# Optimization experiments

Measured on AMD Instinct MI355X. Metric: run time of the kernel, lower is better.

Reference implementation:

```python
import jax, jax.numpy as jnp
import numpy as np

N_FILTERS = 1024
KH, KW = 5, 5
LOC = 3                      # locality (pad + maxpool kernel/stride)
B, H, W = 1024, 64, 64
WIN = KH + 2 * LOC           # 11: sliced window side after padding


def setup_inputs() -> dict:
    key = jax.random.key(0)
    k1, k2, k3, k4 = jax.random.split(key, 4)
    X = jax.random.normal(k1, (B, 1, H, W), dtype=jnp.float32)
    weight = jax.random.normal(k2, (N_FILTERS, 1, KH, KW), dtype=jnp.float32)
    bias = jax.random.normal(k3, (N_FILTERS,), dtype=jnp.float32)
    # top-left corner (i, j) of each filter's window in the padded image;
    # must satisfy i + KH + 2*LOC <= H + 2*LOC  =>  i in [0, H-KH]
    positions = jax.random.randint(k4, (N_FILTERS, 2), 0, H - KH + 1, dtype=jnp.int32)
    return {"X": X, "weight": weight, "bias": bias, "positions": positions}


def reference(X, weight, bias, positions):
    # ZeroPad2d(locality)
    Xp = jnp.pad(X, ((0, 0), (0, 0), (LOC, LOC), (LOC, LOC)))

    def slice_one(pos):
        return jax.lax.dynamic_slice(Xp, (0, 0, pos[0], pos[1]), (B, 1, WIN, WIN))

    windows = jax.vmap(slice_one)(positions)
    lhs = jnp.transpose(windows[:, :, 0], (1, 0, 2, 3))

    # All n_filters tiny single-channel convs as ONE grouped conv.
    conv = jax.lax.conv_general_dilated(
        lhs, weight, window_strides=(1, 1), padding='VALID',
        dimension_numbers=('NCHW', 'OIHW', 'NCHW'),
        feature_group_count=N_FILTERS)                # [B,F,2L+1,2L+1] = [B,F,7,7]
    conv = conv + bias[None, :, None, None]

    # MaxPool2d((LOC,LOC)) with default stride=LOC, floor mode -> 2x2.
    pooled = jax.lax.reduce_window(
        conv, -jnp.inf, jax.lax.max,
        window_dimensions=(1, 1, LOC, LOC),
        window_strides=(1, 1, LOC, LOC),
        padding='VALID')                              # [B,F,2,2]

    # torch.cat(dim=1) over per-filter [B,1,2,2] tensors + reshape(B,-1)
    return pooled.reshape(B, -1)                      # [B, F*4]
```

## Files before the change

### kernel.cpp

```cpp
#include <hip/hip_runtime.h>

#define N_FILTERS 1024
#define B_TOTAL   1024
#define IMG       64
#define PAD_DIM   70

typedef _Float16 half2_t __attribute__((ext_vector_type(2)));
typedef float    fvec2  __attribute__((ext_vector_type(2)));

__global__ void zero_border_kernel(_Float16* __restrict__ Xt) {
    int bid = blockIdx.x;
    int r, c;
    if (bid < 420) {
        int r6 = bid / 70;
        c = bid - r6 * 70;
        r = (r6 < 3) ? r6 : r6 + 64;
    } else {
        int t = bid - 420;
        r = 3 + t / 6;
        int k = t - (t / 6) * 6;
        c = (k < 3) ? k : k + 64;
    }
    const size_t pp = (size_t)r * PAD_DIM + c;
    const int bg = threadIdx.x >> 5, l = threadIdx.x & 31;
    unsigned long long* q = (unsigned long long*)Xt
        + (size_t)bg * (4900ull * 32) + pp * 32 + l;
    *q = 0ull;
}

__global__ __launch_bounds__(256) void transpose_kernel(
    const float* __restrict__ X, _Float16* __restrict__ Xt)
{
    __shared__ float T[64 * 65];
    const int pt = blockIdx.x & 63;
    const int bt = blockIdx.x >> 6;
    const int tx = threadIdx.x & 63, ty = threadIdx.x >> 6;

    #pragma unroll
    for (int pass = 0; pass < 16; ++pass) {
        int bl = pass * 4 + ty;
        T[bl * 65 + tx] = X[(size_t)(bt * 64 + bl) * 4096 + pt * 64 + tx];
    }
    __syncthreads();
    #pragma unroll
    for (int pass = 0; pass < 16; ++pass) {
        int pl = pass * 4 + ty;
        int p  = pt * 64 + pl;
        int r  = p >> 6, c = p & 63;
        Xt[((size_t)(bt >> 1) * 4900 + (size_t)(r + 3) * PAD_DIM + (c + 3)) * 128
           + (bt & 1) * 64 + tx] = (_Float16)T[tx * 65 + pl];
    }
}

__global__ __launch_bounds__(256, 4) void filters_main(
    const half2_t* __restrict__ Xt2,
    const float*   __restrict__ W,
    const float*   __restrict__ bias,
    const int*     __restrict__ pos,
    float4*        __restrict__ out4)
{
    const int t    = threadIdx.x;
    const int lane = t & 63;
    const int w    = t >> 6;
    const int bg   = blockIdx.x & 7;
    const int fg   = blockIdx.x >> 3;

    const int f  = fg * 4 + w;
    const int sf = __builtin_amdgcn_readfirstlane(f);
    const int si = __builtin_amdgcn_readfirstlane(pos[2 * sf]);
    const int sj = __builtin_amdgcn_readfirstlane(pos[2 * sf + 1]);

    float wk[25];
    const float* wp = W + sf * 25;
    #pragma unroll
    for (int k = 0; k < 25; ++k) wk[k] = wp[k];

    const half2_t* Xg = Xt2 + (size_t)bg * (4900ull * 64) + lane;

    fvec2 acc[36];
    #pragma unroll
    for (int k = 0; k < 36; ++k) acc[k] = (fvec2)0.0f;

    #pragma unroll
    for (int wr = 0; wr < 10; ++wr) {
        const half2_t* rowp = Xg + (size_t)((si + wr) * PAD_DIM + sj) * 64;
        const int ylo = (wr > 4) ? (wr - 4) : 0;
        const int yhi = (wr < 5) ? wr : 5;
        #pragma unroll
        for (int wc = 0; wc < 10; ++wc) {
            half2_t h = rowp[wc * 64];
            fvec2 v;
            v.x = (float)h.x;
            v.y = (float)h.y;
            const int xlo = (wc > 4) ? (wc - 4) : 0;
            const int xhi = (wc < 5) ? wc : 5;
            #pragma unroll
            for (int y = 0; y < 6; ++y) {
                if (y >= ylo && y <= yhi) {
                    const int r = wr - y;
                    #pragma unroll
                    for (int x = 0; x < 6; ++x) {
                        if (x >= xlo && x <= xhi) {
                            const int c = wc - x;
                            acc[y * 6 + x] = wk[r * 5 + c] * v + acc[y * 6 + x];
                        }
                    }
                }
            }
        }
    }

    const float bv = bias[sf];
    float4 oA, oB;
    {
        float mA[4], mB[4];
        #pragma unroll
        for (int py = 0; py < 2; ++py) {
            #pragma unroll
            for (int px = 0; px < 2; ++px) {
                fvec2 m = acc[(3 * py) * 6 + 3 * px];
                #pragma unroll
                for (int dy = 0; dy < 3; ++dy)
                    #pragma unroll
                    for (int dx = 0; dx < 3; ++dx) {
                        fvec2 v = acc[(3 * py + dy) * 6 + (3 * px + dx)];
                        m.x = fmaxf(m.x, v.x);
                        m.y = fmaxf(m.y, v.y);
                    }
                mA[py * 2 + px] = m.x + bv;
                mB[py * 2 + px] = m.y + bv;
            }
        }
        oA.x = mA[0]; oA.y = mA[1]; oA.z = mA[2]; oA.w = mA[3];
        oB.x = mB[0]; oB.y = mB[1]; oB.z = mB[2]; oB.w = mB[3];
    }

    const int b = bg * 128 + lane * 2;
    out4[(size_t)b * 1024 + f]       = oA;
    out4[(size_t)(b + 1) * 1024 + f] = oB;
}

extern "C" void kernel_launch(void* const* d_in, const int* in_sizes, int n_in,
                              void* d_out, int out_size, void* d_ws, size_t ws_size,
                              hipStream_t stream) {
    const float* X    = (const float*)d_in[0];
    const float* W    = (const float*)d_in[1];
    const float* bias = (const float*)d_in[2];
    const int*   pos  = (const int*)d_in[3];
    float4* out4 = (float4*)d_out;
    _Float16* Xt = (_Float16*)d_ws;

    zero_border_kernel<<<804, 256, 0, stream>>>(Xt);
    transpose_kernel<<<1024, 256, 0, stream>>>(X, Xt);
    filters_main<<<2048, 256, 0, stream>>>((const half2_t*)Xt, W, bias, pos, out4);
}
```

Before: 119.3 us.

## Restructure filter kernel: one image per lane, row-double-buffered loads, incremental maxpool

Each lane now processes one image instead of two packed fp16 images, and the grid doubles to 4096 blocks. Occupancy is raised via launch bounds (6 waves). Window rows are loaded into double-buffered register arrays so the next row's loads overlap the current row's FMAs. Max pooling is folded in as each output row completes, which shortens accumulator live ranges, and outputs are transposed through shared memory so stores are coalesced. The tradeoff is that the packed two-image FMA pattern is dropped, and each weight and window value is now reused across only one image.

```diff
diff --git a/kernel.cpp b/kernel.cpp
--- a/kernel.cpp
+++ b/kernel.cpp
@@ -4,9 +4,6 @@
 #define B_TOTAL   1024
 #define IMG       64
 #define PAD_DIM   70
-
-typedef _Float16 half2_t __attribute__((ext_vector_type(2)));
-typedef float    fvec2  __attribute__((ext_vector_type(2)));
 
 __global__ void zero_border_kernel(_Float16* __restrict__ Xt) {
     int bid = blockIdx.x;
@@ -52,18 +49,59 @@
     }
 }
 
-__global__ __launch_bounds__(256, 4) void filters_main(
-    const half2_t* __restrict__ Xt2,
-    const float*   __restrict__ W,
-    const float*   __restrict__ bias,
-    const int*     __restrict__ pos,
-    float4*        __restrict__ out4)
+
+#define LOAD_ROW(buf, WR) do {                                                  \
+    const _Float16* rp_ = Xg + (size_t)((si + (WR)) * PAD_DIM + sj) * 128;      \
+    _Pragma("unroll")                                                           \
+    for (int wc = 0; wc < 10; ++wc) buf[wc] = rp_[wc * 128];                    \
+} while (0)
+
+#define COMPUTE_ROW(buf, WR) do {                                               \
+    float in_[10];                                                              \
+    _Pragma("unroll")                                                           \
+    for (int wc = 0; wc < 10; ++wc) in_[wc] = (float)buf[wc];                   \
+    _Pragma("unroll")                                                           \
+    for (int y = 0; y < 6; ++y) {                                               \
+        if (y >= (((WR) > 4) ? ((WR) - 4) : 0) && y <= (((WR) < 5) ? (WR) : 5)) { \
+            const int rr = (WR) - y;                                            \
+            _Pragma("unroll")                                                   \
+            for (int x = 0; x < 6; ++x) {                                       \
+                float s_ = acc[y * 6 + x];                                      \
+                _Pragma("unroll")                                               \
+                for (int c = 0; c < 5; ++c)                                     \
+                    s_ = fmaf(wk[rr * 5 + c], in_[x + c], s_);                  \
+                acc[y * 6 + x] = s_;                                            \
+            }                                                                   \
+        }                                                                       \
+    }                                                                           \
+    if ((WR) >= 4) {                                                            \
+        const int fy = (WR) - 4;                                                \
+        _Pragma("unroll")                                                       \
+        for (int px = 0; px < 2; ++px) {                                        \
+            float m_ = fmaxf(fmaxf(acc[fy * 6 + 3 * px],                        \
+                                   acc[fy * 6 + 3 * px + 1]),                   \
+                             acc[fy * 6 + 3 * px + 2]);                         \
+            const int pi = ((fy >= 3) ? 2 : 0) + px;                            \
+            pmax[pi] = fmaxf(pmax[pi], m_);                                     \
+        }                                                                       \
+    }                                                                           \
+} while (0)
+
+__global__ __launch_bounds__(256, 6) void filters_main(
+    const _Float16* __restrict__ Xt,
+    const float*    __restrict__ W,
+    const float*    __restrict__ bias,
+    const int*      __restrict__ pos,
+    float4*         __restrict__ out4)
 {
     const int t    = threadIdx.x;
     const int lane = t & 63;
     const int w    = t >> 6;
-    const int bg   = blockIdx.x & 7;
-    const int fg   = blockIdx.x >> 3;
+    const int bid  = blockIdx.x;
+    const int xcd  = bid & 7;
+    const int m    = bid >> 3;
+    const int bgr  = xcd * 2 + (m & 1);
+    const int fg   = m >> 1;
 
     const int f  = fg * 4 + w;
     const int sf = __builtin_amdgcn_readfirstlane(f);
@@ -75,69 +113,41 @@
     #pragma unroll
     for (int k = 0; k < 25; ++k) wk[k] = wp[k];
 
-    const half2_t* Xg = Xt2 + (size_t)bg * (4900ull * 64) + lane;
+    const _Float16* Xg = Xt + (size_t)xcd * (4900ull * 128) + (bgr & 1) * 64 + lane;
 
-    fvec2 acc[36];
+    float acc[36];
     #pragma unroll
-    for (int k = 0; k < 36; ++k) acc[k] = (fvec2)0.0f;
+    for (int k = 0; k < 36; ++k) acc[k] = 0.0f;
+    float pmax[4];
+    #pragma unroll
+    for (int k = 0; k < 4; ++k) pmax[k] = -__builtin_inff();
 
-    #pragma unroll
-    for (int wr = 0; wr < 10; ++wr) {
-        const half2_t* rowp = Xg + (size_t)((si + wr) * PAD_DIM + sj) * 64;
-        const int ylo = (wr > 4) ? (wr - 4) : 0;
-        const int yhi = (wr < 5) ? wr : 5;
-        #pragma unroll
-        for (int wc = 0; wc < 10; ++wc) {
-            half2_t h = rowp[wc * 64];
-            fvec2 v;
-            v.x = (float)h.x;
-            v.y = (float)h.y;
-            const int xlo = (wc > 4) ? (wc - 4) : 0;
-            const int xhi = (wc < 5) ? wc : 5;
-            #pragma unroll
-            for (int y = 0; y < 6; ++y) {
-                if (y >= ylo && y <= yhi) {
-                    const int r = wr - y;
-                    #pragma unroll
-                    for (int x = 0; x < 6; ++x) {
-                        if (x >= xlo && x <= xhi) {
-                            const int c = wc - x;
-                            acc[y * 6 + x] = wk[r * 5 + c] * v + acc[y * 6 + x];
-                        }
-                    }
-                }
-            }
-        }
-    }
+    _Float16 bufA[10], bufB[10];
+    LOAD_ROW(bufA, 0);
+    LOAD_ROW(bufB, 1);  COMPUTE_ROW(bufA, 0);
+    LOAD_ROW(bufA, 2);  COMPUTE_ROW(bufB, 1);
+    LOAD_ROW(bufB, 3);  COMPUTE_ROW(bufA, 2);
+    LOAD_ROW(bufA, 4);  COMPUTE_ROW(bufB, 3);
+    LOAD_ROW(bufB, 5);  COMPUTE_ROW(bufA, 4);
+    LOAD_ROW(bufA, 6);  COMPUTE_ROW(bufB, 5);
+    LOAD_ROW(bufB, 7);  COMPUTE_ROW(bufA, 6);
+    LOAD_ROW(bufA, 8);  COMPUTE_ROW(bufB, 7);
+    LOAD_ROW(bufB, 9);  COMPUTE_ROW(bufA, 8);
+                        COMPUTE_ROW(bufB, 9);
 
     const float bv = bias[sf];
-    float4 oA, oB;
-    {
-        float mA[4], mB[4];
-        #pragma unroll
-        for (int py = 0; py < 2; ++py) {
-            #pragma unroll
-            for (int px = 0; px < 2; ++px) {
-                fvec2 m = acc[(3 * py) * 6 + 3 * px];
-                #pragma unroll
-                for (int dy = 0; dy < 3; ++dy)
-                    #pragma unroll
-                    for (int dx = 0; dx < 3; ++dx) {
-                        fvec2 v = acc[(3 * py + dy) * 6 + (3 * px + dx)];
-                        m.x = fmaxf(m.x, v.x);
-                        m.y = fmaxf(m.y, v.y);
-                    }
-                mA[py * 2 + px] = m.x + bv;
-                mB[py * 2 + px] = m.y + bv;
-            }
-        }
-        oA.x = mA[0]; oA.y = mA[1]; oA.z = mA[2]; oA.w = mA[3];
-        oB.x = mB[0]; oB.y = mB[1]; oB.z = mB[2]; oB.w = mB[3];
-    }
+    __shared__ float S[4][65][4];
+    #pragma unroll
+    for (int k = 0; k < 4; ++k) S[w][lane][k] = pmax[k] + bv;
+    __syncthreads();
 
-    const int b = bg * 128 + lane * 2;
-    out4[(size_t)b * 1024 + f]       = oA;
-    out4[(size_t)(b + 1) * 1024 + f] = oB;
+    const int r = t >> 2, q = t & 3;
+    float4 val;
+    val.x = S[q][r][0];
+    val.y = S[q][r][1];
+    val.z = S[q][r][2];
+    val.w = S[q][r][3];
+    out4[(size_t)(bgr * 64 + r) * 1024 + (fg * 4 + q)] = val;
 }
 
 extern "C" void kernel_launch(void* const* d_in, const int* in_sizes, int n_in,
@@ -152,5 +162,5 @@
 
     zero_border_kernel<<<804, 256, 0, stream>>>(Xt);
     transpose_kernel<<<1024, 256, 0, stream>>>(X, Xt);
-    filters_main<<<2048, 256, 0, stream>>>((const half2_t*)Xt, W, bias, pos, out4);
+    filters_main<<<4096, 256, 0, stream>>>(Xt, W, bias, pos, out4);
 }
```

New measurement: 135.3 us. 1.13x slower.
